# Kernel optimization log

Measured on AMD Instinct MI355X. Metric: run time of the kernel, lower is better.

The kernel has to match this reference:

```python
import jax, jax.numpy as jnp
import numpy as np
from jax import lax

B, L, C, P = 512, 6, 4, 45

def _conv(x, w, b, pad):
    y = lax.conv_general_dilated(x, w, (1, 1), [(pad, pad), (pad, pad)],
                                 dimension_numbers=('NCHW', 'OIHW', 'NCHW'))
    return y + b[None, :, None, None]

def _maxpool2(x):
    return lax.reduce_window(x, -jnp.inf, lax.max, (1, 1, 2, 2), (1, 1, 2, 2), 'VALID')

def _prelu(x, a):
    return jnp.where(x >= 0, x, a * x)

def setup_inputs() -> dict:
    key = jax.random.key(0)
    ks = jax.random.split(key, 16)
    s = 0.05
    inp = {
        'x': jax.random.normal(ks[0], (B, L, C, P, P), jnp.float32),
        'w0': jax.random.normal(ks[1], (32, C, 5, 5), jnp.float32) * s,
        'b0': jnp.zeros((32,), jnp.float32),
        'w1': jax.random.normal(ks[2], (32, 32, 5, 5), jnp.float32) * s,
        'b1': jnp.zeros((32,), jnp.float32),
        'w2': jax.random.normal(ks[3], (64, 32, 4, 4), jnp.float32) * s,
        'b2': jnp.zeros((64,), jnp.float32),
        'w3': jax.random.normal(ks[4], (64, 64, 3, 3), jnp.float32) * s,
        'b3': jnp.zeros((64,), jnp.float32),
        'a0': jnp.float32(0.25), 'a1': jnp.float32(0.25),
        'a2': jnp.float32(0.25), 'a3': jnp.float32(0.25),
        'fc1_w': jax.random.normal(ks[5], (L, 256, 128), jnp.float32) * s,
        'fc1_b': jnp.zeros((L, 128), jnp.float32),
        'a4': jnp.full((L, 1), 0.25, jnp.float32),
        'fc2_w': jax.random.normal(ks[6], (L, 128, 64), jnp.float32) * s,
        'fc2_b': jnp.zeros((L, 64), jnp.float32),
        'a5': jnp.full((L, 1), 0.25, jnp.float32),
        'fc3_w': jax.random.normal(ks[7], (L, 64, 4), jnp.float32) * s,
        'fc3_b': jnp.zeros((L, 4), jnp.float32),
    }
    return inp

def reference(x, w0, b0, w1, b1, w2, b2, w3, b3, a0, a1, a2, a3,
              fc1_w, fc1_b, a4, fc2_w, fc2_b, a5, fc3_w, fc3_b):
    b, l = x.shape[0], x.shape[1]
    # Conv tower shares weights across landmarks -> fold landmark into batch.
    h = x.reshape(b * l, x.shape[2], P, P)
    h = _maxpool2(_prelu(_conv(h, w0, b0, 1), a0))   # (BL,32,21,21)
    h = _maxpool2(_prelu(_conv(h, w1, b1, 1), a1))   # (BL,32,9,9)
    h = _maxpool2(_prelu(_conv(h, w2, b2, 1), a2))   # (BL,64,4,4)
    h = _prelu(_conv(h, w3, b3, 0), a3)              # (BL,64,2,2)
    h = h.reshape(b, l, 256)
    # Per-landmark FC heads as batched GEMMs.
    h = _prelu(jnp.einsum('bli,lio->blo', h, fc1_w) + fc1_b, a4)
    h = _prelu(jnp.einsum('bli,lio->blo', h, fc2_w) + fc2_b, a5)
    out = jnp.einsum('bli,lio->blo', h, fc3_w) + fc3_b   # (B,L,4)
    return out
```

## Files before the change

### kernel.cpp

```cpp
#include <hip/hip_runtime.h>
#include <stdint.h>

typedef _Float16 f16;
typedef _Float16 half8 __attribute__((ext_vector_type(8)));
typedef _Float16 half4 __attribute__((ext_vector_type(4)));
typedef float floatx16 __attribute__((ext_vector_type(16)));

#define NIMG 3072

#define WS_W0T   0
#define WS_W1T   10240
#define WS_W2T   61440
#define WS_W3T   126976
#define WS_FC1T  200704
#define WS_FC2T  593920
#define WS_FC3T  692224
#define WS_H3F   16646144

#define Z16 {0.f,0.f,0.f,0.f,0.f,0.f,0.f,0.f,0.f,0.f,0.f,0.f,0.f,0.f,0.f,0.f}

#define TOF(t) ((((t) > 24 ? 24 : (t)) / 5) * 208 + (((t) > 24 ? 24 : (t)) % 5) * 4)

__global__ __launch_bounds__(256) void k_prep(
    const float* __restrict__ w0, const float* __restrict__ w1, const float* __restrict__ w2,
    const float* __restrict__ w3, const float* __restrict__ fc1w, const float* __restrict__ fc2w,
    const float* __restrict__ fc3w,
    f16* __restrict__ w0t, f16* __restrict__ w1t, f16* __restrict__ w2t, f16* __restrict__ w3t,
    f16* __restrict__ fc1t, f16* __restrict__ fc2t, f16* __restrict__ fc3t)
{
  int stride = gridDim.x * blockDim.x;
  int g0 = blockIdx.x * blockDim.x + threadIdx.x;
  for (int i = g0; i < 3584; i += stride) {
    int j = i & 7, co = (i >> 3) & 31, hf = (i >> 8) & 1, t = i >> 9;
    int k = t * 16 + hf * 8 + j, tap = k >> 2, ci = k & 3;
    f16 v = (f16)0.f;
    if (tap < 25) { int ky = tap / 5, kx = tap % 5; v = (f16)w0[((co * 4 + ci) * 5 + ky) * 5 + kx]; }
    w0t[i] = v;
  }
  for (int i = g0; i < 25600; i += stride) {
    int j = i & 7, co = (i >> 3) & 31, hf = (i >> 8) & 1, ch = (i >> 9) & 1, tap = i >> 10;
    int ci = ch * 16 + hf * 8 + j, ky = tap / 5, kx = tap % 5;
    w1t[i] = (f16)w1[((co * 32 + ci) * 5 + ky) * 5 + kx];
  }
  for (int i = g0; i < 32768; i += stride) {
    int j = i & 7, co = (i >> 3) & 31, hf = (i >> 8) & 1, ct = (i >> 9) & 1, ch = (i >> 10) & 1, tap = i >> 11;
    int ci = ch * 16 + hf * 8 + j, cog = ct * 32 + co, ky = tap >> 2, kx = tap & 3;
    w2t[i] = (f16)w2[((cog * 32 + ci) * 4 + ky) * 4 + kx];
  }
  for (int i = g0; i < 36864; i += stride) {
    int j = i & 7, col = (i >> 3) & 31, hf = (i >> 8) & 1, ct = (i >> 9) & 1, c = i >> 10;
    int k = c * 16 + hf * 8 + j, tap = k >> 6, ci = k & 63, co = ct * 32 + col;
    int ky = tap / 3, kx = tap % 3;
    w3t[i] = (f16)w3[((co * 64 + ci) * 3 + ky) * 3 + kx];
  }
  for (int i = g0; i < 196608; i += stride) {
    int j = i & 7, col = (i >> 3) & 31, hf = (i >> 8) & 1, nt = (i >> 9) & 3, c = (i >> 11) & 15, l = i >> 15;
    int k = c * 16 + hf * 8 + j, o = nt * 32 + col;
    fc1t[i] = (f16)fc1w[(l * 256 + k) * 128 + o];
  }
  for (int i = g0; i < 49152; i += stride) {
    int j = i & 7, col = (i >> 3) & 31, hf = (i >> 8) & 1, nt = (i >> 9) & 1, c = (i >> 10) & 7, l = i >> 13;
    int k = c * 16 + hf * 8 + j, o = nt * 32 + col;
    fc2t[i] = (f16)fc2w[(l * 128 + k) * 64 + o];
  }
  for (int i = g0; i < 12288; i += stride) {
    int j = i & 7, col = (i >> 3) & 31, hf = (i >> 8) & 1, c = (i >> 9) & 3, l = i >> 11;
    int k = c * 16 + hf * 8 + j;
    f16 v = (f16)0.f;
    if (col < 4) v = (f16)fc3w[(l * 64 + k) * 4 + col];
    fc3t[i] = v;
  }
}

__global__ __launch_bounds__(512) void k_conv012(
    const float* __restrict__ x,
    const f16* __restrict__ w0t, const float* __restrict__ b0, const float* __restrict__ a0p,
    const f16* __restrict__ w1t, const float* __restrict__ b1, const float* __restrict__ a1p,
    const f16* __restrict__ w2t, const float* __restrict__ b2, const float* __restrict__ a2p,
    f16* __restrict__ h3f)
{
  __shared__ __align__(16) uint32_t smem_u[16328];
  f16* sh   = (f16*)smem_u;
  f16* s_x  = sh;
  f16* s_h1 = sh + 9776;

  const int n = blockIdx.x, tid = threadIdx.x;
  const int wv = tid >> 6, l = tid & 63;
  const int hf = l >> 5, m = l & 31, dr = m >> 3, dc = m & 7, col = m;
  const float a0 = a0p[0], a1 = a1p[0];
  const float b0c = b0[col], b1c = b1[col];
  const half8* w0t8 = (const half8*)w0t;
  const half8* w1t8 = (const half8*)w1t;
  const half8* w2t8 = (const half8*)w2t;

  for (int i = tid; i < 734; i += 512) {
    int w;
    if (i < 104) w = i;
    else { int j = i - 104; int r = j / 14 + 1, c = j % 14; w = r * 104 + (c < 2 ? c : 90 + c); }
    smem_u[w] = 0u;
  }
  for (int i = tid; i < 2096; i += 512) {
    int cell = i >> 4, wi = i & 15, r, c;
    if (cell < 26) { r = 0; c = cell; }
    else { int j = cell - 26; r = j / 5 + 1; int c5 = j % 5; c = (c5 == 0) ? 0 : 21 + c5; }
    smem_u[4888 + (r * 26 + c) * 20 + wi] = 0u;
  }
  const float* xin = x + n * 8100;
  for (int p = tid; p < 2025; p += 512) {
    int y = p / 45, xx = p % 45;
    half4 h;
    h[0] = (f16)xin[p];
    h[1] = (f16)xin[p + 2025];
    h[2] = (f16)xin[p + 4050];
    h[3] = (f16)xin[p + 6075];
    *(half4*)(s_x + ((y + 1) * 52 + (xx + 1)) * 4) = h;
  }
  __syncthreads();

  half8 B0[7];
  #pragma unroll
  for (int q = 0; q < 7; ++q)
    B0[q] = w0t8[(q * 2 + hf) * 32 + col];

  const int cdr = (m & 1) | ((m & 8) >> 2);
  const int cdc = ((m >> 1) & 3) | ((m & 16) >> 2);
  for (int t = wv; t < 66; t += 8) {
    int g = t / 6;
    int r0 = 4 * g; if (r0 > 38) r0 = 38;
    int cb = (t % 6) * 8;
    int rowb = r0 + cdr, colb = cb + cdc;
    const f16* base = s_x + (rowb * 52 + colb) * 4;
    floatx16 acc = Z16;
    #pragma unroll
    for (int q = 0; q < 7; ++q) {
      const int offL = hf ? TOF(4 * q + 2) : TOF(4 * q);
      half4 lo = *(const half4*)(base + offL);
      half4 hi;
      if (q < 6) {
        const int offH = hf ? TOF(4 * q + 3) : TOF(4 * q + 1);
        hi = *(const half4*)(base + offH);
      } else {
        hi = (half4){(f16)0, (f16)0, (f16)0, (f16)0};
      }
      half8 av = __builtin_shufflevector(lo, hi, 0, 1, 2, 3, 4, 5, 6, 7);
      acc = __builtin_amdgcn_mfma_f32_32x32x16_f16(av, B0[q], acc, 0, 0, 0);
    }
    #pragma unroll
    for (int q = 0; q < 4; ++q) {
      float v = fmaxf(fmaxf(acc[4*q], acc[4*q + 1]), fmaxf(acc[4*q + 2], acc[4*q + 3]));
      v += b0c; v = (v >= 0.f) ? v : a0 * v;
      int pr = (r0 >> 1) + (q & 1), pc = (cb >> 1) + hf + 2 * (q >> 1);
      if (pc < 21) s_h1[((pr + 1) * 26 + (pc + 1)) * 40 + col] = (f16)v;
    }
  }
  __syncthreads();

  for (int i = tid; i < 640; i += 512) {
    int cell = i >> 4, wi = i & 15, r, c;
    if (cell < 11)      { r = 0;  c = cell; }
    else if (cell < 22) { r = 10; c = cell - 11; }
    else if (cell < 31) { r = cell - 21; c = 0; }
    else                { r = cell - 30; c = 10; }
    smem_u[(r * 12 + c) * 20 + wi] = 0u;
  }

  int t0 = wv * 2;
  int t1 = t0 + 1; if (t1 > 14) t1 = 14;
  int r0a = 4 * (t0 / 3); if (r0a > 14) r0a = 14;
  int cca = 8 * (t0 % 3); if (cca > 14) cca = 14;
  int r0b = 4 * (t1 / 3); if (r0b > 14) r0b = 14;
  int ccb = 8 * (t1 % 3); if (ccb > 14) ccb = 14;
  const f16* pAa = s_h1 + ((r0a + dr) * 26 + cca + dc) * 40 + hf * 8;
  const f16* pAb = s_h1 + ((r0b + dr) * 26 + ccb + dc) * 40 + hf * 8;
  floatx16 accA = Z16;
  floatx16 accB = Z16;
  for (int ky = 0; ky < 5; ++ky) {
    const half8* wb = w1t8 + ky * 640 + hf * 32 + col;
    const f16* qa = pAa + ky * 1040;
    const f16* qb = pAb + ky * 1040;
    #pragma unroll
    for (int kx = 0; kx < 5; ++kx) {
      #pragma unroll
      for (int ch = 0; ch < 2; ++ch) {
        half8 b  = wb[kx * 128 + ch * 64];
        half8 aA = *(const half8*)(qa + kx * 40 + ch * 16);
        half8 aB = *(const half8*)(qb + kx * 40 + ch * 16);
        accA = __builtin_amdgcn_mfma_f32_32x32x16_f16(aA, b, accA, 0, 0, 0);
        accB = __builtin_amdgcn_mfma_f32_32x32x16_f16(aB, b, accB, 0, 0, 0);
      }
    }
  }
  __syncthreads();

  f16* s2 = s_x;
  #pragma unroll
  for (int tt = 0; tt < 2; ++tt) {
    const floatx16 acc = tt ? accB : accA;
    int r0 = tt ? r0b : r0a, cc = tt ? ccb : cca;
    #pragma unroll
    for (int pp = 0; pp < 2; ++pp)
      #pragma unroll
      for (int c2 = 0; c2 < 2; ++c2) {
        float v = fmaxf(fmaxf(acc[8*pp + 2*c2], acc[8*pp + 2*c2 + 1]),
                        fmaxf(acc[8*pp + 4 + 2*c2], acc[8*pp + 4 + 2*c2 + 1]));
        v += b1c; v = (v >= 0.f) ? v : a1 * v;
        int pr = (r0 >> 1) + pp, pc = (cc >> 1) + 2 * hf + c2;
        if (pc < 9) s2[((pr + 1) * 12 + (pc + 1)) * 40 + col] = (f16)v;
      }
  }
  __syncthreads();

  if (wv < 4) {
    const int mt = wv >> 1, c2t = wv & 1;
    const float a2 = a2p[0];
    const float b2c = b2[c2t * 32 + col];
    const f16* pA = s2 + ((mt * 4 + dr) * 12 + dc) * 40 + hf * 8;
    floatx16 acc = Z16;
    #pragma unroll 4
    for (int tap = 0; tap < 16; ++tap) {
      int aoff = ((tap >> 2) * 12 + (tap & 3)) * 40;
      #pragma unroll
      for (int ch = 0; ch < 2; ++ch) {
        half8 b = w2t8[tap * 256 + ch * 128 + c2t * 64 + hf * 32 + col];
        half8 a = *(const half8*)(pA + aoff + ch * 16);
        acc = __builtin_amdgcn_mfma_f32_32x32x16_f16(a, b, acc, 0, 0, 0);
      }
    }
    f16* o = h3f + n * 1024;
    #pragma unroll
    for (int pp = 0; pp < 2; ++pp)
      #pragma unroll
      for (int c2 = 0; c2 < 2; ++c2) {
        float v = fmaxf(fmaxf(acc[8*pp + 2*c2], acc[8*pp + 2*c2 + 1]),
                        fmaxf(acc[8*pp + 4 + 2*c2], acc[8*pp + 4 + 2*c2 + 1]));
        v += b2c; v = (v >= 0.f) ? v : a2 * v;
        int pr = mt * 2 + pp, pc = 2 * hf + c2;
        o[(pr * 4 + pc) * 64 + c2t * 32 + col] = (f16)v;
      }
  }
}

__global__ __launch_bounds__(256) void k_tail(
    const f16* __restrict__ h3f,
    const f16* __restrict__ w3t, const float* __restrict__ b3, const float* __restrict__ a3p,
    const f16* __restrict__ fc1t, const float* __restrict__ fc1b, const float* __restrict__ a4,
    const f16* __restrict__ fc2t, const float* __restrict__ fc2b, const float* __restrict__ a5,
    const f16* __restrict__ fc3t, const float* __restrict__ fc3b,
    float* __restrict__ out)
{
  __shared__ __align__(16) f16 s_feat[32 * 264];
  __shared__ __align__(16) f16 s_g1[32 * 136];
  __shared__ __align__(16) f16 s_g2[32 * 72];

  const int lm = blockIdx.x % 6, t = blockIdx.x / 6;
  const int tid = threadIdx.x, wv = tid >> 6, lane = tid & 63;
  const int hf = lane >> 5, col = lane & 31;
  const half8* w3t8  = (const half8*)w3t;
  const half8* fc1t8 = (const half8*)fc1t;
  const half8* fc2t8 = (const half8*)fc2t;
  const half8* fc3t8 = (const half8*)fc3t;

  {
    const int mt = wv;
    const int i_img = mt * 8 + (col >> 2);
    const int pos = col & 3, oy = pos >> 1, ox = pos & 1;
    const int gimg = (t * 32 + i_img) * 6 + lm;
    const f16* Abase = h3f + gimg * 1024 + (oy * 4 + ox) * 64;
    floatx16 acc0 = Z16, acc1 = Z16;
    for (int c = 0; c < 36; ++c) {
      int tap = c >> 2;
      int ky = tap / 3, kx = tap % 3;
      half8 a = *(const half8*)(Abase + (ky * 4 + kx) * 64 + (c & 3) * 16 + hf * 8);
      half8 bb0 = w3t8[((c * 2 + 0) * 2 + hf) * 32 + col];
      half8 bb1 = w3t8[((c * 2 + 1) * 2 + hf) * 32 + col];
      acc0 = __builtin_amdgcn_mfma_f32_32x32x16_f16(a, bb0, acc0, 0, 0, 0);
      acc1 = __builtin_amdgcn_mfma_f32_32x32x16_f16(a, bb1, acc1, 0, 0, 0);
    }
    const float a3 = a3p[0];
    #pragma unroll
    for (int ct = 0; ct < 2; ++ct) {
      const floatx16 acc = ct ? acc1 : acc0;
      const int co = ct * 32 + col;
      const float bb = b3[co];
      #pragma unroll
      for (int q = 0; q < 4; ++q) {
        int ii = mt * 8 + 2 * q + hf;
        half4 w;
        #pragma unroll
        for (int z = 0; z < 4; ++z) {
          float v = acc[q * 4 + z] + bb;
          v = (v >= 0.f) ? v : a3 * v;
          w[z] = (f16)v;
        }
        *(half4*)(s_feat + ii * 264 + co * 4) = w;
      }
    }
  }
  __syncthreads();

  {
    floatx16 g = Z16;
    for (int c = 0; c < 16; ++c) {
      half8 a = *(const half8*)(s_feat + col * 264 + c * 16 + hf * 8);
      half8 b = fc1t8[(((lm * 16 + c) * 4 + wv) * 2 + hf) * 32 + col];
      g = __builtin_amdgcn_mfma_f32_32x32x16_f16(a, b, g, 0, 0, 0);
    }
    const float a4v = a4[lm];
    const float bb = fc1b[lm * 128 + wv * 32 + col];
    #pragma unroll
    for (int reg = 0; reg < 16; ++reg) {
      int r = (reg & 3) + 8 * (reg >> 2) + 4 * hf;
      float v = g[reg] + bb;
      v = (v >= 0.f) ? v : a4v * v;
      s_g1[r * 136 + wv * 32 + col] = (f16)v;
    }
  }
  __syncthreads();

  if (wv < 2) {
    floatx16 g = Z16;
    for (int c = 0; c < 8; ++c) {
      half8 a = *(const half8*)(s_g1 + col * 136 + c * 16 + hf * 8);
      half8 b = fc2t8[(((lm * 8 + c) * 2 + wv) * 2 + hf) * 32 + col];
      g = __builtin_amdgcn_mfma_f32_32x32x16_f16(a, b, g, 0, 0, 0);
    }
    const float a5v = a5[lm];
    const float bb = fc2b[lm * 64 + wv * 32 + col];
    #pragma unroll
    for (int reg = 0; reg < 16; ++reg) {
      int r = (reg & 3) + 8 * (reg >> 2) + 4 * hf;
      float v = g[reg] + bb;
      v = (v >= 0.f) ? v : a5v * v;
      s_g2[r * 72 + wv * 32 + col] = (f16)v;
    }
  }
  __syncthreads();

  if (wv == 0) {
    floatx16 g = Z16;
    for (int c = 0; c < 4; ++c) {
      half8 a = *(const half8*)(s_g2 + col * 72 + c * 16 + hf * 8);
      half8 b = fc3t8[((lm * 4 + c) * 2 + hf) * 32 + col];
      g = __builtin_amdgcn_mfma_f32_32x32x16_f16(a, b, g, 0, 0, 0);
    }
    if (col < 4) {
      const float bb = fc3b[lm * 4 + col];
      #pragma unroll
      for (int reg = 0; reg < 16; ++reg) {
        int r = (reg & 3) + 8 * (reg >> 2) + 4 * hf;
        out[((t * 32 + r) * 6 + lm) * 4 + col] = g[reg] + bb;
      }
    }
  }
}

extern "C" void kernel_launch(void* const* d_in, const int* in_sizes, int n_in,
                              void* d_out, int out_size, void* d_ws, size_t ws_size,
                              hipStream_t stream) {
  const float* x    = (const float*)d_in[0];
  const float* w0   = (const float*)d_in[1];
  const float* b0   = (const float*)d_in[2];
  const float* w1   = (const float*)d_in[3];
  const float* b1   = (const float*)d_in[4];
  const float* w2   = (const float*)d_in[5];
  const float* b2   = (const float*)d_in[6];
  const float* w3   = (const float*)d_in[7];
  const float* b3   = (const float*)d_in[8];
  const float* a0   = (const float*)d_in[9];
  const float* a1   = (const float*)d_in[10];
  const float* a2   = (const float*)d_in[11];
  const float* a3   = (const float*)d_in[12];
  const float* fc1w = (const float*)d_in[13];
  const float* fc1b = (const float*)d_in[14];
  const float* a4   = (const float*)d_in[15];
  const float* fc2w = (const float*)d_in[16];
  const float* fc2b = (const float*)d_in[17];
  const float* a5   = (const float*)d_in[18];
  const float* fc3w = (const float*)d_in[19];
  const float* fc3b = (const float*)d_in[20];
  float* out = (float*)d_out;

  char* ws = (char*)d_ws;
  f16* w0t  = (f16*)(ws + WS_W0T);
  f16* w1t  = (f16*)(ws + WS_W1T);
  f16* w2t  = (f16*)(ws + WS_W2T);
  f16* w3t  = (f16*)(ws + WS_W3T);
  f16* fc1t = (f16*)(ws + WS_FC1T);
  f16* fc2t = (f16*)(ws + WS_FC2T);
  f16* fc3t = (f16*)(ws + WS_FC3T);
  f16* h3f  = (f16*)(ws + WS_H3F);

  k_prep   <<<128, 256, 0, stream>>>(w0, w1, w2, w3, fc1w, fc2w, fc3w,
                                     w0t, w1t, w2t, w3t, fc1t, fc2t, fc3t);
  k_conv012<<<NIMG, 512, 0, stream>>>(x, w0t, b0, a0, w1t, b1, a1, w2t, b2, a2, h3f);
  k_tail   <<<96, 256, 0, stream>>>(h3f, w3t, b3, a3, fc1t, fc1b, a4,
                                    fc2t, fc2b, a5, fc3t, fc3b, out);
}
```

Baseline: 318.6 us.

## Stream conv0 input in row bands to shrink shared memory footprint

Loads the input image into LDS in three overlapping row bands and runs conv0 per band, instead of staging the whole padded image at once. The input buffer is placed after the h1 buffer and reuses its space, which cuts the total LDS allocation, and padding zeros are written during the band loads. The goal is more resident blocks per CU, at the cost of extra barriers and reloading the halo rows between bands.

```diff
diff --git a/kernel.cpp b/kernel.cpp
--- a/kernel.cpp
+++ b/kernel.cpp
@@ -79,10 +79,10 @@
     const f16* __restrict__ w2t, const float* __restrict__ b2, const float* __restrict__ a2p,
     f16* __restrict__ h3f)
 {
-  __shared__ __align__(16) uint32_t smem_u[16328];
+  __shared__ __align__(16) uint32_t smem_u[13520];
   f16* sh   = (f16*)smem_u;
-  f16* s_x  = sh;
-  f16* s_h1 = sh + 9776;
+  f16* s_h1 = sh;
+  f16* s_x  = sh + 22880;
 
   const int n = blockIdx.x, tid = threadIdx.x;
   const int wv = tid >> 6, l = tid & 63;
@@ -93,29 +93,12 @@
   const half8* w1t8 = (const half8*)w1t;
   const half8* w2t8 = (const half8*)w2t;
 
-  for (int i = tid; i < 734; i += 512) {
-    int w;
-    if (i < 104) w = i;
-    else { int j = i - 104; int r = j / 14 + 1, c = j % 14; w = r * 104 + (c < 2 ? c : 90 + c); }
-    smem_u[w] = 0u;
-  }
   for (int i = tid; i < 2096; i += 512) {
     int cell = i >> 4, wi = i & 15, r, c;
     if (cell < 26) { r = 0; c = cell; }
     else { int j = cell - 26; r = j / 5 + 1; int c5 = j % 5; c = (c5 == 0) ? 0 : 21 + c5; }
-    smem_u[4888 + (r * 26 + c) * 20 + wi] = 0u;
-  }
-  const float* xin = x + n * 8100;
-  for (int p = tid; p < 2025; p += 512) {
-    int y = p / 45, xx = p % 45;
-    half4 h;
-    h[0] = (f16)xin[p];
-    h[1] = (f16)xin[p + 2025];
-    h[2] = (f16)xin[p + 4050];
-    h[3] = (f16)xin[p + 6075];
-    *(half4*)(s_x + ((y + 1) * 52 + (xx + 1)) * 4) = h;
-  }
-  __syncthreads();
+    smem_u[(r * 26 + c) * 20 + wi] = 0u;
+  }
 
   half8 B0[7];
   #pragma unroll
@@ -124,44 +107,56 @@
 
   const int cdr = (m & 1) | ((m & 8) >> 2);
   const int cdc = ((m >> 1) & 3) | ((m & 16) >> 2);
-  for (int t = wv; t < 66; t += 8) {
-    int g = t / 6;
-    int r0 = 4 * g; if (r0 > 38) r0 = 38;
-    int cb = (t % 6) * 8;
-    int rowb = r0 + cdr, colb = cb + cdc;
-    const f16* base = s_x + (rowb * 52 + colb) * 4;
-    floatx16 acc = Z16;
-    #pragma unroll
-    for (int q = 0; q < 7; ++q) {
-      const int offL = hf ? TOF(4 * q + 2) : TOF(4 * q);
-      half4 lo = *(const half4*)(base + offL);
-      half4 hi;
-      if (q < 6) {
-        const int offH = hf ? TOF(4 * q + 3) : TOF(4 * q + 1);
-        hi = *(const half4*)(base + offH);
-      } else {
-        hi = (half4){(f16)0, (f16)0, (f16)0, (f16)0};
-      }
-      half8 av = __builtin_shufflevector(lo, hi, 0, 1, 2, 3, 4, 5, 6, 7);
-      acc = __builtin_amdgcn_mfma_f32_32x32x16_f16(av, B0[q], acc, 0, 0, 0);
-    }
-    #pragma unroll
-    for (int q = 0; q < 4; ++q) {
-      float v = fmaxf(fmaxf(acc[4*q], acc[4*q + 1]), fmaxf(acc[4*q + 2], acc[4*q + 3]));
-      v += b0c; v = (v >= 0.f) ? v : a0 * v;
-      int pr = (r0 >> 1) + (q & 1), pc = (cb >> 1) + hf + 2 * (q >> 1);
-      if (pc < 21) s_h1[((pr + 1) * 26 + (pc + 1)) * 40 + col] = (f16)v;
-    }
-  }
-  __syncthreads();
-
-  for (int i = tid; i < 640; i += 512) {
-    int cell = i >> 4, wi = i & 15, r, c;
-    if (cell < 11)      { r = 0;  c = cell; }
-    else if (cell < 22) { r = 10; c = cell - 11; }
-    else if (cell < 31) { r = cell - 21; c = 0; }
-    else                { r = cell - 30; c = 10; }
-    smem_u[(r * 12 + c) * 20 + wi] = 0u;
+  const float* xin = x + n * 8100;
+
+  #pragma unroll
+  for (int band = 0; band < 3; ++band) {
+    const int lo = band * 16;
+    const int nrows = (band < 2) ? 20 : 14;
+    const int t1b = (band < 2) ? band * 24 + 24 : 66;
+    for (int i = tid; i < nrows * 52; i += 512) {
+      int rp = lo + i / 52, cp = i % 52;
+      half4 h = {(f16)0, (f16)0, (f16)0, (f16)0};
+      if (rp >= 1 && cp >= 1 && cp <= 45) {
+        const float* px = xin + (rp - 1) * 45 + (cp - 1);
+        h[0] = (f16)px[0];
+        h[1] = (f16)px[2025];
+        h[2] = (f16)px[4050];
+        h[3] = (f16)px[6075];
+      }
+      *(half4*)(s_x + ((rp - lo) * 52 + cp) * 4) = h;
+    }
+    __syncthreads();
+    for (int t = band * 24 + wv; t < t1b; t += 8) {
+      int g = t / 6;
+      int r0 = 4 * g; if (r0 > 38) r0 = 38;
+      int cb = (t % 6) * 8;
+      int rowb = r0 - lo + cdr, colb = cb + cdc;
+      const f16* base = s_x + (rowb * 52 + colb) * 4;
+      floatx16 acc = Z16;
+      #pragma unroll
+      for (int q = 0; q < 7; ++q) {
+        const int offL = hf ? TOF(4 * q + 2) : TOF(4 * q);
+        half4 lo4 = *(const half4*)(base + offL);
+        half4 hi4;
+        if (q < 6) {
+          const int offH = hf ? TOF(4 * q + 3) : TOF(4 * q + 1);
+          hi4 = *(const half4*)(base + offH);
+        } else {
+          hi4 = (half4){(f16)0, (f16)0, (f16)0, (f16)0};
+        }
+        half8 av = __builtin_shufflevector(lo4, hi4, 0, 1, 2, 3, 4, 5, 6, 7);
+        acc = __builtin_amdgcn_mfma_f32_32x32x16_f16(av, B0[q], acc, 0, 0, 0);
+      }
+      #pragma unroll
+      for (int q = 0; q < 4; ++q) {
+        float v = fmaxf(fmaxf(acc[4*q], acc[4*q + 1]), fmaxf(acc[4*q + 2], acc[4*q + 3]));
+        v += b0c; v = (v >= 0.f) ? v : a0 * v;
+        int pr = (r0 >> 1) + (q & 1), pc = (cb >> 1) + hf + 2 * (q >> 1);
+        if (pc < 21) s_h1[((pr + 1) * 26 + (pc + 1)) * 40 + col] = (f16)v;
+      }
+    }
+    __syncthreads();
   }
 
   int t0 = wv * 2;
@@ -192,7 +187,15 @@
   }
   __syncthreads();
 
-  f16* s2 = s_x;
+  f16* s2 = sh;
+  for (int i = tid; i < 640; i += 512) {
+    int cell = i >> 4, wi = i & 15, r, c;
+    if (cell < 11)      { r = 0;  c = cell; }
+    else if (cell < 22) { r = 10; c = cell - 11; }
+    else if (cell < 31) { r = cell - 21; c = 0; }
+    else                { r = cell - 30; c = 10; }
+    smem_u[(r * 12 + c) * 20 + wi] = 0u;
+  }
   #pragma unroll
   for (int tt = 0; tt < 2; ++tt) {
     const floatx16 acc = tt ? accB : accA;
```

Result: slower. 326.6 us (+2.5%).

## Retile conv1 by pooled output cells to cut redundant MFMA work

Applied to the files above, without the earlier changes.

Conv1 used to be tiled as 15 overlapping 4x8 spatial tiles, clamped at the edges, with two accumulators per wave. Each tile now covers 8 pooled cells times 4 quad positions, so the 81 pooled outputs fit in 11 tiles with almost no overlap. Pooling is done in registers before the store. The padded stride of the second activation buffer changes from 12 to 14, which keeps the border zeroing and the conv2 addressing consistent. The trade is an imbalance: only 3 waves run a second tile, which loses the interleaving of two independent MFMA chains.

```diff
diff --git a/kernel.cpp b/kernel.cpp
--- a/kernel.cpp
+++ b/kernel.cpp
@@ -134,15 +134,15 @@
     #pragma unroll
     for (int q = 0; q < 7; ++q) {
       const int offL = hf ? TOF(4 * q + 2) : TOF(4 * q);
-      half4 lo = *(const half4*)(base + offL);
-      half4 hi;
+      half4 lo4 = *(const half4*)(base + offL);
+      half4 hi4;
       if (q < 6) {
         const int offH = hf ? TOF(4 * q + 3) : TOF(4 * q + 1);
-        hi = *(const half4*)(base + offH);
+        hi4 = *(const half4*)(base + offH);
       } else {
-        hi = (half4){(f16)0, (f16)0, (f16)0, (f16)0};
-      }
-      half8 av = __builtin_shufflevector(lo, hi, 0, 1, 2, 3, 4, 5, 6, 7);
+        hi4 = (half4){(f16)0, (f16)0, (f16)0, (f16)0};
+      }
+      half8 av = __builtin_shufflevector(lo4, hi4, 0, 1, 2, 3, 4, 5, 6, 7);
       acc = __builtin_amdgcn_mfma_f32_32x32x16_f16(av, B0[q], acc, 0, 0, 0);
     }
     #pragma unroll
@@ -161,52 +161,59 @@
     else if (cell < 22) { r = 10; c = cell - 11; }
     else if (cell < 31) { r = cell - 21; c = 0; }
     else                { r = cell - 30; c = 10; }
-    smem_u[(r * 12 + c) * 20 + wi] = 0u;
-  }
-
-  int t0 = wv * 2;
-  int t1 = t0 + 1; if (t1 > 14) t1 = 14;
-  int r0a = 4 * (t0 / 3); if (r0a > 14) r0a = 14;
-  int cca = 8 * (t0 % 3); if (cca > 14) cca = 14;
-  int r0b = 4 * (t1 / 3); if (r0b > 14) r0b = 14;
-  int ccb = 8 * (t1 % 3); if (ccb > 14) ccb = 14;
-  const f16* pAa = s_h1 + ((r0a + dr) * 26 + cca + dc) * 40 + hf * 8;
-  const f16* pAb = s_h1 + ((r0b + dr) * 26 + ccb + dc) * 40 + hf * 8;
-  floatx16 accA = Z16;
-  floatx16 accB = Z16;
-  for (int ky = 0; ky < 5; ++ky) {
-    const half8* wb = w1t8 + ky * 640 + hf * 32 + col;
-    const f16* qa = pAa + ky * 1040;
-    const f16* qb = pAb + ky * 1040;
-    #pragma unroll
-    for (int kx = 0; kx < 5; ++kx) {
+    smem_u[(r * 14 + c) * 20 + wi] = 0u;
+  }
+
+  const int q_ = m & 3, gcell = m >> 2;
+  auto conv1_tile = [&](int t) -> half4 {
+    int e = 8 * t + gcell; if (e > 80) e = 80;
+    int er = (e * 57) >> 9, ec = e - 9 * er;
+    int rm = 2 * er + (q_ >> 1), cm = 2 * ec + (q_ & 1);
+    const f16* pA = s_h1 + (rm * 26 + cm) * 40 + hf * 8;
+    floatx16 acc = Z16;
+    for (int ky = 0; ky < 5; ++ky) {
+      const half8* wb = w1t8 + ky * 640 + hf * 32 + col;
+      const f16* qa = pA + ky * 1040;
       #pragma unroll
-      for (int ch = 0; ch < 2; ++ch) {
-        half8 b  = wb[kx * 128 + ch * 64];
-        half8 aA = *(const half8*)(qa + kx * 40 + ch * 16);
-        half8 aB = *(const half8*)(qb + kx * 40 + ch * 16);
-        accA = __builtin_amdgcn_mfma_f32_32x32x16_f16(aA, b, accA, 0, 0, 0);
-        accB = __builtin_amdgcn_mfma_f32_32x32x16_f16(aB, b, accB, 0, 0, 0);
-      }
-    }
-  }
+      for (int kx = 0; kx < 5; ++kx) {
+        #pragma unroll
+        for (int ch = 0; ch < 2; ++ch) {
+          half8 b = wb[kx * 128 + ch * 64];
+          half8 a = *(const half8*)(qa + kx * 40 + ch * 16);
+          acc = __builtin_amdgcn_mfma_f32_32x32x16_f16(a, b, acc, 0, 0, 0);
+        }
+      }
+    }
+    half4 w;
+    #pragma unroll
+    for (int u = 0; u < 4; ++u) {
+      float v = fmaxf(fmaxf(acc[4*u], acc[4*u + 1]), fmaxf(acc[4*u + 2], acc[4*u + 3]));
+      v += b1c; v = (v >= 0.f) ? v : a1 * v;
+      w[u] = (f16)v;
+    }
+    return w;
+  };
+  half4 wr0 = conv1_tile(wv);
+  half4 wr1 = {(f16)0, (f16)0, (f16)0, (f16)0};
+  if (wv < 3) wr1 = conv1_tile(8 + wv);
   __syncthreads();
 
   f16* s2 = s_x;
   #pragma unroll
-  for (int tt = 0; tt < 2; ++tt) {
-    const floatx16 acc = tt ? accB : accA;
-    int r0 = tt ? r0b : r0a, cc = tt ? ccb : cca;
-    #pragma unroll
-    for (int pp = 0; pp < 2; ++pp)
-      #pragma unroll
-      for (int c2 = 0; c2 < 2; ++c2) {
-        float v = fmaxf(fmaxf(acc[8*pp + 2*c2], acc[8*pp + 2*c2 + 1]),
-                        fmaxf(acc[8*pp + 4 + 2*c2], acc[8*pp + 4 + 2*c2 + 1]));
-        v += b1c; v = (v >= 0.f) ? v : a1 * v;
-        int pr = (r0 >> 1) + pp, pc = (cc >> 1) + 2 * hf + c2;
-        if (pc < 9) s2[((pr + 1) * 12 + (pc + 1)) * 40 + col] = (f16)v;
-      }
+  for (int u = 0; u < 4; ++u) {
+    int e = 8 * wv + 2 * u + hf;
+    int er = (e * 57) >> 9, ec = e - 9 * er;
+    s2[((er + 1) * 14 + (ec + 1)) * 40 + col] = wr0[u];
+  }
+  if (wv < 3) {
+    #pragma unroll
+    for (int u = 0; u < 4; ++u) {
+      int e = 8 * (8 + wv) + 2 * u + hf;
+      if (e <= 80) {
+        int er = (e * 57) >> 9, ec = e - 9 * er;
+        s2[((er + 1) * 14 + (ec + 1)) * 40 + col] = wr1[u];
+      }
+    }
   }
   __syncthreads();
 
@@ -214,11 +221,11 @@
     const int mt = wv >> 1, c2t = wv & 1;
     const float a2 = a2p[0];
     const float b2c = b2[c2t * 32 + col];
-    const f16* pA = s2 + ((mt * 4 + dr) * 12 + dc) * 40 + hf * 8;
+    const f16* pA = s2 + ((mt * 4 + dr) * 14 + dc) * 40 + hf * 8;
     floatx16 acc = Z16;
     #pragma unroll 4
     for (int tap = 0; tap < 16; ++tap) {
-      int aoff = ((tap >> 2) * 12 + (tap & 3)) * 40;
+      int aoff = ((tap >> 2) * 14 + (tap & 3)) * 40;
       #pragma unroll
       for (int ch = 0; ch < 2; ++ch) {
         half8 b = w2t8[tap * 256 + ch * 128 + c2t * 64 + hf * 32 + col];
```

Result: slower. 335.9 us (+5.4%).
